# Optimization experiments

Measured on AMD Instinct MI355X. Metric: run time of the kernel, lower is better.

The kernel has to match this reference:

```python
import jax, jax.numpy as jnp
import numpy as np

T, B, DIM, LATENT, OUT = 512, 1024, 128, 256, 64


def setup_inputs() -> dict:
    key = jax.random.key(0)
    ks = jax.random.split(key, 6)
    s_i = 1.0 / np.sqrt(DIM)
    s_h = 1.0 / np.sqrt(LATENT)
    return {
        "x": jax.random.normal(ks[0], (T, B, DIM), dtype=jnp.float32),
        "h": jnp.zeros((B, LATENT), dtype=jnp.float32),
        "Wi": jax.random.uniform(ks[1], (DIM, LATENT), jnp.float32, -s_i, s_i),
        "bi": jax.random.uniform(ks[2], (LATENT,), jnp.float32, -s_i, s_i),
        "Wh": jax.random.uniform(ks[3], (LATENT, LATENT), jnp.float32, -s_h, s_h),
        "Wd": jax.random.uniform(ks[4], (LATENT, OUT), jnp.float32, -s_h, s_h),
        "bd": jax.random.uniform(ks[5], (OUT,), jnp.float32, -s_h, s_h),
    }


def reference(x, h, Wi, bi, Wh, Wd, bd):
    # Precompute input projections for all steps in one big GEMM: [T,B,latent]
    xi = jnp.einsum("tbd,dl->tbl", x, Wi) + bi

    def step(h, xi_t):
        h = jnp.tanh(xi_t + h @ Wh)
        return h, None

    h_final, _ = jax.lax.scan(step, h, xi)
    return jax.nn.sigmoid(h_final @ Wd + bd)
```

## Files before the change

### kernel.cpp

```cpp
#include <hip/hip_runtime.h>
#include <cmath>
#include <cstdint>

constexpr int T_STEPS = 512;
constexpr int BATCH   = 1024;
constexpr int DIM     = 128;
constexpr int LATENT  = 256;
constexpr int OUT_DIM = 64;
constexpr int ROWS    = 16;

typedef __attribute__((ext_vector_type(8))) short bf16x8;
typedef __attribute__((ext_vector_type(4))) float f32x4;
typedef __attribute__((ext_vector_type(4))) int   i32x4;

__device__ __forceinline__ uint32_t f2bf(float f) {
    uint32_t u = __builtin_bit_cast(uint32_t, f);
    return (u + 0x7FFFu + ((u >> 16) & 1u)) >> 16;
}
__device__ __forceinline__ uint32_t pk2(float a, float b) {
    return f2bf(a) | (f2bf(b) << 16);
}
__device__ __forceinline__ float fast_tanh(float v) {
    float e = __builtin_amdgcn_exp2f(v * 2.885390081777927f);
    return __builtin_fmaf(-2.0f, __builtin_amdgcn_rcpf(e + 1.0f), 1.0f);
}
__device__ __forceinline__ float fast_sigmoid(float v) {
    float e = __builtin_amdgcn_exp2f(v * -1.4426950408889634f);
    return __builtin_amdgcn_rcpf(e + 1.0f);
}
__device__ __forceinline__ int q8(float v, float inv) {
    return (int)__builtin_rintf(v * inv);
}
__device__ __forceinline__ uint32_t pack4(int a, int b, int c, int d) {
    return (uint32_t)(a & 255) | ((uint32_t)(b & 255) << 8) |
           ((uint32_t)(c & 255) << 16) | ((uint32_t)(d & 255) << 24);
}
__device__ __forceinline__ int swz(int sl, int b) {
    return (sl ^ (b & 3) ^ ((b >> 2) & 3)) & 3;
}

__global__ __launch_bounds__(512)
void rnn_i8h(const float* __restrict__ x,
             const float* __restrict__ h0,
             const float* __restrict__ Wi,
             const float* __restrict__ bi,
             const float* __restrict__ Wh,
             const float* __restrict__ Wd,
             const float* __restrict__ bd,
             float* __restrict__ out)
{
    __shared__ __align__(16) uint8_t hls[2][4096];
    __shared__ __align__(16) uint8_t xls[2][4096];

    const int tid  = threadIdx.x;
    const int lane = tid & 63;
    const int wv   = tid >> 6;
    const int b0   = blockIdx.x * ROWS;
    const int b15  = lane & 15;
    const int kgrp = lane >> 4;
    const int tg0  = wv * 2, tg1 = wv * 2 + 1;
    const int wcol0 = tg0 * 16 + b15;
    const int wcol1 = wcol0 + 16;

    float cmh0 = 0.f, cmh1 = 0.f;
    {
        const float* p0 = Wh + (size_t)(kgrp * 16) * LATENT + wcol0;
        #pragma unroll 4
        for (int i = 0; i < 64; ++i) {
            const size_t off = (size_t)((i >> 4) * 64 + (i & 15)) * LATENT;
            cmh0 = fmaxf(cmh0, fabsf(p0[off]));
            cmh1 = fmaxf(cmh1, fabsf(p0[off + 16]));
        }
        cmh0 = fmaxf(cmh0, __shfl_xor(cmh0, 16));
        cmh0 = fmaxf(cmh0, __shfl_xor(cmh0, 32));
        cmh1 = fmaxf(cmh1, __shfl_xor(cmh1, 16));
        cmh1 = fmaxf(cmh1, __shfl_xor(cmh1, 32));
    }
    const float ih0 = cmh0 > 0.f ? 127.f / cmh0 : 0.f;
    const float ih1 = cmh1 > 0.f ? 127.f / cmh1 : 0.f;

#define WHQ(J) q8(_p[(size_t)(J) * LATENT], _inv)
#define LOADWH(NAME, WC, S, INV)                                            \
    i32x4 NAME; {                                                           \
        const float* _p = Wh + (size_t)((S) * 64 + kgrp * 16) * LATENT + (WC); \
        const float _inv = (INV);                                           \
        NAME[0] = (int)pack4(WHQ(0),  WHQ(1),  WHQ(2),  WHQ(3));            \
        NAME[1] = (int)pack4(WHQ(4),  WHQ(5),  WHQ(6),  WHQ(7));            \
        NAME[2] = (int)pack4(WHQ(8),  WHQ(9),  WHQ(10), WHQ(11));           \
        NAME[3] = (int)pack4(WHQ(12), WHQ(13), WHQ(14), WHQ(15));           \
    }
    LOADWH(AH0_0, wcol0, 0, ih0) LOADWH(AH0_1, wcol0, 1, ih0)
    LOADWH(AH0_2, wcol0, 2, ih0) LOADWH(AH0_3, wcol0, 3, ih0)
    LOADWH(AH1_0, wcol1, 0, ih1) LOADWH(AH1_1, wcol1, 1, ih1)
    LOADWH(AH1_2, wcol1, 2, ih1) LOADWH(AH1_3, wcol1, 3, ih1)

#define LOADWX(NAME, WC, S)                                                 \
    bf16x8 NAME; {                                                          \
        const float* _p = Wi + (size_t)((S) * 32 + kgrp * 8) * LATENT + (WC); \
        NAME[0] = (short)f2bf(_p[0]);                                       \
        NAME[1] = (short)f2bf(_p[(size_t)1 * LATENT]);                      \
        NAME[2] = (short)f2bf(_p[(size_t)2 * LATENT]);                      \
        NAME[3] = (short)f2bf(_p[(size_t)3 * LATENT]);                      \
        NAME[4] = (short)f2bf(_p[(size_t)4 * LATENT]);                      \
        NAME[5] = (short)f2bf(_p[(size_t)5 * LATENT]);                      \
        NAME[6] = (short)f2bf(_p[(size_t)6 * LATENT]);                      \
        NAME[7] = (short)f2bf(_p[(size_t)7 * LATENT]);                      \
    }
    LOADWX(AX0_0, wcol0, 0) LOADWX(AX0_1, wcol0, 1)
    LOADWX(AX0_2, wcol0, 2) LOADWX(AX0_3, wcol0, 3)
    LOADWX(AX1_0, wcol1, 0) LOADWX(AX1_1, wcol1, 1)
    LOADWX(AX1_2, wcol1, 2) LOADWX(AX1_3, wcol1, 3)

    const float dh0_0 = __shfl(cmh0, kgrp * 4 + 0) * (1.f / 16129.f);
    const float dh0_1 = __shfl(cmh0, kgrp * 4 + 1) * (1.f / 16129.f);
    const float dh0_2 = __shfl(cmh0, kgrp * 4 + 2) * (1.f / 16129.f);
    const float dh0_3 = __shfl(cmh0, kgrp * 4 + 3) * (1.f / 16129.f);
    const float dh1_0 = __shfl(cmh1, kgrp * 4 + 0) * (1.f / 16129.f);
    const float dh1_1 = __shfl(cmh1, kgrp * 4 + 1) * (1.f / 16129.f);
    const float dh1_2 = __shfl(cmh1, kgrp * 4 + 2) * (1.f / 16129.f);
    const float dh1_3 = __shfl(cmh1, kgrp * 4 + 3) * (1.f / 16129.f);
    const float cb0_0 = bi[tg0 * 16 + kgrp * 4 + 0];
    const float cb0_1 = bi[tg0 * 16 + kgrp * 4 + 1];
    const float cb0_2 = bi[tg0 * 16 + kgrp * 4 + 2];
    const float cb0_3 = bi[tg0 * 16 + kgrp * 4 + 3];
    const float cb1_0 = bi[tg1 * 16 + kgrp * 4 + 0];
    const float cb1_1 = bi[tg1 * 16 + kgrp * 4 + 1];
    const float cb1_2 = bi[tg1 * 16 + kgrp * 4 + 2];
    const float cb1_3 = bi[tg1 * 16 + kgrp * 4 + 3];

    const int pr = tid & 15;
    const int pq = tid >> 4;
    const int stb = (pq >> 3) * 1024 + pr * 64 +
                    (swz((pq >> 1) & 3, pr) << 4) + (pq & 1) * 8;
    {
        const float* hp = h0 + (size_t)(b0 + pr) * LATENT + pq * 8;
        uint32_t u0 = pack4(q8(hp[0], 127.f), q8(hp[1], 127.f),
                            q8(hp[2], 127.f), q8(hp[3], 127.f));
        uint32_t u1 = pack4(q8(hp[4], 127.f), q8(hp[5], 127.f),
                            q8(hp[6], 127.f), q8(hp[7], 127.f));
        *reinterpret_cast<uint2*>(&hls[0][stb]) = make_uint2(u0, u1);
        const float* xq = x + (size_t)(b0 + pr) * DIM + pq * 4;
        float4 xv = *reinterpret_cast<const float4*>(xq);
        *reinterpret_cast<uint2*>(&xls[0][stb]) =
            make_uint2(pk2(xv.x, xv.y), pk2(xv.z, xv.w));
    }
    __syncthreads();

    const int hrd = b15 * 64 + (swz(kgrp, b15) << 4);
    const int wb0 = (tg0 >> 2) * 1024 + b15 * 64 +
                    (swz(tg0 & 3, b15) << 4) + kgrp * 4;
    const int wb1 = (tg1 >> 2) * 1024 + b15 * 64 +
                    (swz(tg1 & 3, b15) << 4) + kgrp * 4;
    const float* xp = x + ((size_t)BATCH + b0 + pr) * DIM + pq * 4;

    int cur = 0;
    for (int t = 0; t < T_STEPS; ++t) {
        const bool pf = (t + 1 < T_STEPS);
        float4 xv;
        if (pf) {
            xv = *reinterpret_cast<const float4*>(xp);
            xp += (size_t)BATCH * DIM;
        }

        const uint8_t* hb = &hls[cur][hrd];
        const uint8_t* xb = &xls[cur][hrd];
        i32x4  bh0 = *reinterpret_cast<const i32x4*>(hb);
        i32x4  bh1 = *reinterpret_cast<const i32x4*>(hb + 1024);
        i32x4  bh2 = *reinterpret_cast<const i32x4*>(hb + 2048);
        i32x4  bh3 = *reinterpret_cast<const i32x4*>(hb + 3072);
        bf16x8 bx0 = *reinterpret_cast<const bf16x8*>(xb);
        bf16x8 bx1 = *reinterpret_cast<const bf16x8*>(xb + 1024);
        bf16x8 bx2 = *reinterpret_cast<const bf16x8*>(xb + 2048);
        bf16x8 bx3 = *reinterpret_cast<const bf16x8*>(xb + 3072);

        i32x4 ch0 = {0, 0, 0, 0}, ch1 = {0, 0, 0, 0};
        f32x4 cx0 = {cb0_0, cb0_1, cb0_2, cb0_3};
        f32x4 cx1 = {cb1_0, cb1_1, cb1_2, cb1_3};

        ch0 = __builtin_amdgcn_mfma_i32_16x16x64_i8(AH0_0, bh0, ch0, 0, 0, 0);
        ch1 = __builtin_amdgcn_mfma_i32_16x16x64_i8(AH1_0, bh0, ch1, 0, 0, 0);
        cx0 = __builtin_amdgcn_mfma_f32_16x16x32_bf16(AX0_0, bx0, cx0, 0, 0, 0);
        cx1 = __builtin_amdgcn_mfma_f32_16x16x32_bf16(AX1_0, bx0, cx1, 0, 0, 0);
        ch0 = __builtin_amdgcn_mfma_i32_16x16x64_i8(AH0_1, bh1, ch0, 0, 0, 0);
        ch1 = __builtin_amdgcn_mfma_i32_16x16x64_i8(AH1_1, bh1, ch1, 0, 0, 0);
        cx0 = __builtin_amdgcn_mfma_f32_16x16x32_bf16(AX0_1, bx1, cx0, 0, 0, 0);
        cx1 = __builtin_amdgcn_mfma_f32_16x16x32_bf16(AX1_1, bx1, cx1, 0, 0, 0);
        ch0 = __builtin_amdgcn_mfma_i32_16x16x64_i8(AH0_2, bh2, ch0, 0, 0, 0);
        ch1 = __builtin_amdgcn_mfma_i32_16x16x64_i8(AH1_2, bh2, ch1, 0, 0, 0);
        cx0 = __builtin_amdgcn_mfma_f32_16x16x32_bf16(AX0_2, bx2, cx0, 0, 0, 0);
        cx1 = __builtin_amdgcn_mfma_f32_16x16x32_bf16(AX1_2, bx2, cx1, 0, 0, 0);
        ch0 = __builtin_amdgcn_mfma_i32_16x16x64_i8(AH0_3, bh3, ch0, 0, 0, 0);
        ch1 = __builtin_amdgcn_mfma_i32_16x16x64_i8(AH1_3, bh3, ch1, 0, 0, 0);
        cx0 = __builtin_amdgcn_mfma_f32_16x16x32_bf16(AX0_3, bx3, cx0, 0, 0, 0);
        cx1 = __builtin_amdgcn_mfma_f32_16x16x32_bf16(AX1_3, bx3, cx1, 0, 0, 0);

        const int nxt = cur ^ 1;
        {
            float v0 = fast_tanh(__builtin_fmaf((float)ch0[0], dh0_0, cx0[0]));
            float v1 = fast_tanh(__builtin_fmaf((float)ch0[1], dh0_1, cx0[1]));
            float v2 = fast_tanh(__builtin_fmaf((float)ch0[2], dh0_2, cx0[2]));
            float v3 = fast_tanh(__builtin_fmaf((float)ch0[3], dh0_3, cx0[3]));
            *reinterpret_cast<uint32_t*>(&hls[nxt][wb0]) =
                pack4(q8(v0, 127.f), q8(v1, 127.f), q8(v2, 127.f), q8(v3, 127.f));
        }
        {
            float v0 = fast_tanh(__builtin_fmaf((float)ch1[0], dh1_0, cx1[0]));
            float v1 = fast_tanh(__builtin_fmaf((float)ch1[1], dh1_1, cx1[1]));
            float v2 = fast_tanh(__builtin_fmaf((float)ch1[2], dh1_2, cx1[2]));
            float v3 = fast_tanh(__builtin_fmaf((float)ch1[3], dh1_3, cx1[3]));
            *reinterpret_cast<uint32_t*>(&hls[nxt][wb1]) =
                pack4(q8(v0, 127.f), q8(v1, 127.f), q8(v2, 127.f), q8(v3, 127.f));
        }
        if (pf)
            *reinterpret_cast<uint2*>(&xls[nxt][stb]) =
                make_uint2(pk2(xv.x, xv.y), pk2(xv.z, xv.w));

        __syncthreads();
        cur = nxt;
    }

    {
        const int o  = tid & 63;
        const int rb = tid >> 6;
        float s0 = 0.f, s1 = 0.f;
        #pragma unroll 4
        for (int k = 0; k < LATENT; k += 4) {
            const int sl   = (k >> 4) & 3;
            const int base = (k >> 6) * 1024 + (k & 15);
            const uint32_t pA = *reinterpret_cast<const uint32_t*>(
                &hls[cur][base + rb * 64 + (swz(sl, rb) << 4)]);
            const uint32_t pB = *reinterpret_cast<const uint32_t*>(
                &hls[cur][base + (rb + 8) * 64 + (swz(sl, rb + 8) << 4)]);
            const float w0 = Wd[(size_t)(k + 0) * OUT_DIM + o];
            const float w1 = Wd[(size_t)(k + 1) * OUT_DIM + o];
            const float w2 = Wd[(size_t)(k + 2) * OUT_DIM + o];
            const float w3 = Wd[(size_t)(k + 3) * OUT_DIM + o];
            s0 += (float)(int8_t)(pA) * w0 + (float)(int8_t)(pA >> 8) * w1
                + (float)(int8_t)(pA >> 16) * w2 + (float)(int8_t)(pA >> 24) * w3;
            s1 += (float)(int8_t)(pB) * w0 + (float)(int8_t)(pB >> 8) * w1
                + (float)(int8_t)(pB >> 16) * w2 + (float)(int8_t)(pB >> 24) * w3;
        }
        out[(size_t)(b0 + rb) * OUT_DIM + o] =
            fast_sigmoid(bd[o] + s0 * (1.f / 127.f));
        out[(size_t)(b0 + rb + 8) * OUT_DIM + o] =
            fast_sigmoid(bd[o] + s1 * (1.f / 127.f));
    }
}

extern "C" void kernel_launch(void* const* d_in, const int* in_sizes, int n_in,
                              void* d_out, int out_size, void* d_ws, size_t ws_size,
                              hipStream_t stream) {
    const float* x  = (const float*)d_in[0];
    const float* h0 = (const float*)d_in[1];
    const float* Wi = (const float*)d_in[2];
    const float* bi = (const float*)d_in[3];
    const float* Wh = (const float*)d_in[4];
    const float* Wd = (const float*)d_in[5];
    const float* bd = (const float*)d_in[6];
    float* out = (float*)d_out;

    hipLaunchKernelGGL(rnn_i8h, dim3(BATCH / ROWS), dim3(512), 0, stream,
                       x, h0, Wi, bi, Wh, Wd, bd, out);
}
```

Measured before the change: 402.8 us.

## Quantize input projection to int8 MFMA and use an LDS-only barrier

Replaces the bf16 x·Wi MFMAs with int8 MFMAs. Wi is quantized per column, and x is clamped to about ±3.97 and quantized with a fixed scale of 32. This halves the x-side MFMA count and LDS traffic on each recurrent step, with dequantization folded into the FMA before tanh. The per-step __syncthreads is replaced by a barrier that waits only on LDS counters, so the prefetch of the next x from global memory is not stalled. The cost is lower accuracy: the fixed x range assumes roughly unit-scale inputs and clips anything outside it.

```diff
diff --git a/kernel.cpp b/kernel.cpp
--- a/kernel.cpp
+++ b/kernel.cpp
@@ -9,17 +9,9 @@
 constexpr int OUT_DIM = 64;
 constexpr int ROWS    = 16;
 
-typedef __attribute__((ext_vector_type(8))) short bf16x8;
 typedef __attribute__((ext_vector_type(4))) float f32x4;
 typedef __attribute__((ext_vector_type(4))) int   i32x4;
 
-__device__ __forceinline__ uint32_t f2bf(float f) {
-    uint32_t u = __builtin_bit_cast(uint32_t, f);
-    return (u + 0x7FFFu + ((u >> 16) & 1u)) >> 16;
-}
-__device__ __forceinline__ uint32_t pk2(float a, float b) {
-    return f2bf(a) | (f2bf(b) << 16);
-}
 __device__ __forceinline__ float fast_tanh(float v) {
     float e = __builtin_amdgcn_exp2f(v * 2.885390081777927f);
     return __builtin_fmaf(-2.0f, __builtin_amdgcn_rcpf(e + 1.0f), 1.0f);
@@ -31,6 +23,9 @@
 __device__ __forceinline__ int q8(float v, float inv) {
     return (int)__builtin_rintf(v * inv);
 }
+__device__ __forceinline__ int q8x(float v) {
+    return (int)__builtin_rintf(fminf(fmaxf(v, -3.96875f), 3.96875f) * 32.f);
+}
 __device__ __forceinline__ uint32_t pack4(int a, int b, int c, int d) {
     return (uint32_t)(a & 255) | ((uint32_t)(b & 255) << 8) |
            ((uint32_t)(c & 255) << 16) | ((uint32_t)(d & 255) << 24);
@@ -38,19 +33,35 @@
 __device__ __forceinline__ int swz(int sl, int b) {
     return (sl ^ (b & 3) ^ ((b >> 2) & 3)) & 3;
 }
+__device__ __forceinline__ void barrier_lds_only() {
+    asm volatile("s_waitcnt lgkmcnt(0)" ::: "memory");
+    __builtin_amdgcn_s_barrier();
+    asm volatile("" ::: "memory");
+}
+
+#define WQJ(J) q8(_p[(size_t)(J) * LATENT], _inv)
+#define LOADQ(NAME, MAT, WC, S, INV)                                        \
+    i32x4 NAME; {                                                           \
+        const float* _p = (MAT) + (size_t)((S) * 64 + kgrp * 16) * LATENT + (WC); \
+        const float _inv = (INV);                                           \
+        NAME[0] = (int)pack4(WQJ(0),  WQJ(1),  WQJ(2),  WQJ(3));            \
+        NAME[1] = (int)pack4(WQJ(4),  WQJ(5),  WQJ(6),  WQJ(7));            \
+        NAME[2] = (int)pack4(WQJ(8),  WQJ(9),  WQJ(10), WQJ(11));           \
+        NAME[3] = (int)pack4(WQJ(12), WQJ(13), WQJ(14), WQJ(15));           \
+    }
 
 __global__ __launch_bounds__(512)
-void rnn_i8h(const float* __restrict__ x,
-             const float* __restrict__ h0,
-             const float* __restrict__ Wi,
-             const float* __restrict__ bi,
-             const float* __restrict__ Wh,
-             const float* __restrict__ Wd,
-             const float* __restrict__ bd,
-             float* __restrict__ out)
+void rnn_i8hx(const float* __restrict__ x,
+              const float* __restrict__ h0,
+              const float* __restrict__ Wi,
+              const float* __restrict__ bi,
+              const float* __restrict__ Wh,
+              const float* __restrict__ Wd,
+              const float* __restrict__ bd,
+              float* __restrict__ out)
 {
     __shared__ __align__(16) uint8_t hls[2][4096];
-    __shared__ __align__(16) uint8_t xls[2][4096];
+    __shared__ __align__(16) uint8_t xls[2][2048];
 
     const int tid  = threadIdx.x;
     const int lane = tid & 63;
@@ -62,7 +73,7 @@
     const int wcol0 = tg0 * 16 + b15;
     const int wcol1 = wcol0 + 16;
 
-    float cmh0 = 0.f, cmh1 = 0.f;
+    float cmh0 = 0.f, cmh1 = 0.f, cmx0 = 0.f, cmx1 = 0.f;
     {
         const float* p0 = Wh + (size_t)(kgrp * 16) * LATENT + wcol0;
         #pragma unroll 4
@@ -71,45 +82,33 @@
             cmh0 = fmaxf(cmh0, fabsf(p0[off]));
             cmh1 = fmaxf(cmh1, fabsf(p0[off + 16]));
         }
+        const float* q0 = Wi + (size_t)(kgrp * 16) * LATENT + wcol0;
+        #pragma unroll 4
+        for (int i = 0; i < 32; ++i) {
+            const size_t off = (size_t)((i >> 4) * 64 + (i & 15)) * LATENT;
+            cmx0 = fmaxf(cmx0, fabsf(q0[off]));
+            cmx1 = fmaxf(cmx1, fabsf(q0[off + 16]));
+        }
         cmh0 = fmaxf(cmh0, __shfl_xor(cmh0, 16));
         cmh0 = fmaxf(cmh0, __shfl_xor(cmh0, 32));
         cmh1 = fmaxf(cmh1, __shfl_xor(cmh1, 16));
         cmh1 = fmaxf(cmh1, __shfl_xor(cmh1, 32));
+        cmx0 = fmaxf(cmx0, __shfl_xor(cmx0, 16));
+        cmx0 = fmaxf(cmx0, __shfl_xor(cmx0, 32));
+        cmx1 = fmaxf(cmx1, __shfl_xor(cmx1, 16));
+        cmx1 = fmaxf(cmx1, __shfl_xor(cmx1, 32));
     }
     const float ih0 = cmh0 > 0.f ? 127.f / cmh0 : 0.f;
     const float ih1 = cmh1 > 0.f ? 127.f / cmh1 : 0.f;
-
-#define WHQ(J) q8(_p[(size_t)(J) * LATENT], _inv)
-#define LOADWH(NAME, WC, S, INV)                                            \
-    i32x4 NAME; {                                                           \
-        const float* _p = Wh + (size_t)((S) * 64 + kgrp * 16) * LATENT + (WC); \
-        const float _inv = (INV);                                           \
-        NAME[0] = (int)pack4(WHQ(0),  WHQ(1),  WHQ(2),  WHQ(3));            \
-        NAME[1] = (int)pack4(WHQ(4),  WHQ(5),  WHQ(6),  WHQ(7));            \
-        NAME[2] = (int)pack4(WHQ(8),  WHQ(9),  WHQ(10), WHQ(11));           \
-        NAME[3] = (int)pack4(WHQ(12), WHQ(13), WHQ(14), WHQ(15));           \
-    }
-    LOADWH(AH0_0, wcol0, 0, ih0) LOADWH(AH0_1, wcol0, 1, ih0)
-    LOADWH(AH0_2, wcol0, 2, ih0) LOADWH(AH0_3, wcol0, 3, ih0)
-    LOADWH(AH1_0, wcol1, 0, ih1) LOADWH(AH1_1, wcol1, 1, ih1)
-    LOADWH(AH1_2, wcol1, 2, ih1) LOADWH(AH1_3, wcol1, 3, ih1)
-
-#define LOADWX(NAME, WC, S)                                                 \
-    bf16x8 NAME; {                                                          \
-        const float* _p = Wi + (size_t)((S) * 32 + kgrp * 8) * LATENT + (WC); \
-        NAME[0] = (short)f2bf(_p[0]);                                       \
-        NAME[1] = (short)f2bf(_p[(size_t)1 * LATENT]);                      \
-        NAME[2] = (short)f2bf(_p[(size_t)2 * LATENT]);                      \
-        NAME[3] = (short)f2bf(_p[(size_t)3 * LATENT]);                      \
-        NAME[4] = (short)f2bf(_p[(size_t)4 * LATENT]);                      \
-        NAME[5] = (short)f2bf(_p[(size_t)5 * LATENT]);                      \
-        NAME[6] = (short)f2bf(_p[(size_t)6 * LATENT]);                      \
-        NAME[7] = (short)f2bf(_p[(size_t)7 * LATENT]);                      \
-    }
-    LOADWX(AX0_0, wcol0, 0) LOADWX(AX0_1, wcol0, 1)
-    LOADWX(AX0_2, wcol0, 2) LOADWX(AX0_3, wcol0, 3)
-    LOADWX(AX1_0, wcol1, 0) LOADWX(AX1_1, wcol1, 1)
-    LOADWX(AX1_2, wcol1, 2) LOADWX(AX1_3, wcol1, 3)
+    const float ix0 = cmx0 > 0.f ? 127.f / cmx0 : 0.f;
+    const float ix1 = cmx1 > 0.f ? 127.f / cmx1 : 0.f;
+
+    LOADQ(AH0_0, Wh, wcol0, 0, ih0) LOADQ(AH0_1, Wh, wcol0, 1, ih0)
+    LOADQ(AH0_2, Wh, wcol0, 2, ih0) LOADQ(AH0_3, Wh, wcol0, 3, ih0)
+    LOADQ(AH1_0, Wh, wcol1, 0, ih1) LOADQ(AH1_1, Wh, wcol1, 1, ih1)
+    LOADQ(AH1_2, Wh, wcol1, 2, ih1) LOADQ(AH1_3, Wh, wcol1, 3, ih1)
+    LOADQ(AX0_0, Wi, wcol0, 0, ix0) LOADQ(AX0_1, Wi, wcol0, 1, ix0)
+    LOADQ(AX1_0, Wi, wcol1, 0, ix1) LOADQ(AX1_1, Wi, wcol1, 1, ix1)
 
     const float dh0_0 = __shfl(cmh0, kgrp * 4 + 0) * (1.f / 16129.f);
     const float dh0_1 = __shfl(cmh0, kgrp * 4 + 1) * (1.f / 16129.f);
@@ -119,6 +118,14 @@
     const float dh1_1 = __shfl(cmh1, kgrp * 4 + 1) * (1.f / 16129.f);
     const float dh1_2 = __shfl(cmh1, kgrp * 4 + 2) * (1.f / 16129.f);
     const float dh1_3 = __shfl(cmh1, kgrp * 4 + 3) * (1.f / 16129.f);
+    const float dx0_0 = __shfl(cmx0, kgrp * 4 + 0) * (1.f / 4064.f);
+    const float dx0_1 = __shfl(cmx0, kgrp * 4 + 1) * (1.f / 4064.f);
+    const float dx0_2 = __shfl(cmx0, kgrp * 4 + 2) * (1.f / 4064.f);
+    const float dx0_3 = __shfl(cmx0, kgrp * 4 + 3) * (1.f / 4064.f);
+    const float dx1_0 = __shfl(cmx1, kgrp * 4 + 0) * (1.f / 4064.f);
+    const float dx1_1 = __shfl(cmx1, kgrp * 4 + 1) * (1.f / 4064.f);
+    const float dx1_2 = __shfl(cmx1, kgrp * 4 + 2) * (1.f / 4064.f);
+    const float dx1_3 = __shfl(cmx1, kgrp * 4 + 3) * (1.f / 4064.f);
     const float cb0_0 = bi[tg0 * 16 + kgrp * 4 + 0];
     const float cb0_1 = bi[tg0 * 16 + kgrp * 4 + 1];
     const float cb0_2 = bi[tg0 * 16 + kgrp * 4 + 2];
@@ -132,6 +139,8 @@
     const int pq = tid >> 4;
     const int stb = (pq >> 3) * 1024 + pr * 64 +
                     (swz((pq >> 1) & 3, pr) << 4) + (pq & 1) * 8;
+    const int stbx = (pq >> 4) * 1024 + pr * 64 +
+                     (swz((pq >> 2) & 3, pr) << 4) + (pq & 3) * 4;
     {
         const float* hp = h0 + (size_t)(b0 + pr) * LATENT + pq * 8;
         uint32_t u0 = pack4(q8(hp[0], 127.f), q8(hp[1], 127.f),
@@ -141,8 +150,8 @@
         *reinterpret_cast<uint2*>(&hls[0][stb]) = make_uint2(u0, u1);
         const float* xq = x + (size_t)(b0 + pr) * DIM + pq * 4;
         float4 xv = *reinterpret_cast<const float4*>(xq);
-        *reinterpret_cast<uint2*>(&xls[0][stb]) =
-            make_uint2(pk2(xv.x, xv.y), pk2(xv.z, xv.w));
+        *reinterpret_cast<uint32_t*>(&xls[0][stbx]) =
+            pack4(q8x(xv.x), q8x(xv.y), q8x(xv.z), q8x(xv.w));
     }
     __syncthreads();
 
@@ -161,61 +170,60 @@
             xv = *reinterpret_cast<const float4*>(xp);
             xp += (size_t)BATCH * DIM;
         }
-
         const uint8_t* hb = &hls[cur][hrd];
         const uint8_t* xb = &xls[cur][hrd];
-        i32x4  bh0 = *reinterpret_cast<const i32x4*>(hb);
-        i32x4  bh1 = *reinterpret_cast<const i32x4*>(hb + 1024);
-        i32x4  bh2 = *reinterpret_cast<const i32x4*>(hb + 2048);
-        i32x4  bh3 = *reinterpret_cast<const i32x4*>(hb + 3072);
-        bf16x8 bx0 = *reinterpret_cast<const bf16x8*>(xb);
-        bf16x8 bx1 = *reinterpret_cast<const bf16x8*>(xb + 1024);
-        bf16x8 bx2 = *reinterpret_cast<const bf16x8*>(xb + 2048);
-        bf16x8 bx3 = *reinterpret_cast<const bf16x8*>(xb + 3072);
+        i32x4 bh0 = *reinterpret_cast<const i32x4*>(hb);
+        i32x4 bh1 = *reinterpret_cast<const i32x4*>(hb + 1024);
+        i32x4 bh2 = *reinterpret_cast<const i32x4*>(hb + 2048);
+        i32x4 bh3 = *reinterpret_cast<const i32x4*>(hb + 3072);
+        i32x4 bx0 = *reinterpret_cast<const i32x4*>(xb);
+        i32x4 bx1 = *reinterpret_cast<const i32x4*>(xb + 1024);
 
         i32x4 ch0 = {0, 0, 0, 0}, ch1 = {0, 0, 0, 0};
-        f32x4 cx0 = {cb0_0, cb0_1, cb0_2, cb0_3};
-        f32x4 cx1 = {cb1_0, cb1_1, cb1_2, cb1_3};
-
+        i32x4 cx0 = {0, 0, 0, 0}, cx1 = {0, 0, 0, 0};
         ch0 = __builtin_amdgcn_mfma_i32_16x16x64_i8(AH0_0, bh0, ch0, 0, 0, 0);
         ch1 = __builtin_amdgcn_mfma_i32_16x16x64_i8(AH1_0, bh0, ch1, 0, 0, 0);
-        cx0 = __builtin_amdgcn_mfma_f32_16x16x32_bf16(AX0_0, bx0, cx0, 0, 0, 0);
-        cx1 = __builtin_amdgcn_mfma_f32_16x16x32_bf16(AX1_0, bx0, cx1, 0, 0, 0);
+        cx0 = __builtin_amdgcn_mfma_i32_16x16x64_i8(AX0_0, bx0, cx0, 0, 0, 0);
+        cx1 = __builtin_amdgcn_mfma_i32_16x16x64_i8(AX1_0, bx0, cx1, 0, 0, 0);
         ch0 = __builtin_amdgcn_mfma_i32_16x16x64_i8(AH0_1, bh1, ch0, 0, 0, 0);
         ch1 = __builtin_amdgcn_mfma_i32_16x16x64_i8(AH1_1, bh1, ch1, 0, 0, 0);
-        cx0 = __builtin_amdgcn_mfma_f32_16x16x32_bf16(AX0_1, bx1, cx0, 0, 0, 0);
-        cx1 = __builtin_amdgcn_mfma_f32_16x16x32_bf16(AX1_1, bx1, cx1, 0, 0, 0);
+        cx0 = __builtin_amdgcn_mfma_i32_16x16x64_i8(AX0_1, bx1, cx0, 0, 0, 0);
+        cx1 = __builtin_amdgcn_mfma_i32_16x16x64_i8(AX1_1, bx1, cx1, 0, 0, 0);
         ch0 = __builtin_amdgcn_mfma_i32_16x16x64_i8(AH0_2, bh2, ch0, 0, 0, 0);
         ch1 = __builtin_amdgcn_mfma_i32_16x16x64_i8(AH1_2, bh2, ch1, 0, 0, 0);
-        cx0 = __builtin_amdgcn_mfma_f32_16x16x32_bf16(AX0_2, bx2, cx0, 0, 0, 0);
-        cx1 = __builtin_amdgcn_mfma_f32_16x16x32_bf16(AX1_2, bx2, cx1, 0, 0, 0);
         ch0 = __builtin_amdgcn_mfma_i32_16x16x64_i8(AH0_3, bh3, ch0, 0, 0, 0);
         ch1 = __builtin_amdgcn_mfma_i32_16x16x64_i8(AH1_3, bh3, ch1, 0, 0, 0);
-        cx0 = __builtin_amdgcn_mfma_f32_16x16x32_bf16(AX0_3, bx3, cx0, 0, 0, 0);
-        cx1 = __builtin_amdgcn_mfma_f32_16x16x32_bf16(AX1_3, bx3, cx1, 0, 0, 0);
 
         const int nxt = cur ^ 1;
         {
-            float v0 = fast_tanh(__builtin_fmaf((float)ch0[0], dh0_0, cx0[0]));
-            float v1 = fast_tanh(__builtin_fmaf((float)ch0[1], dh0_1, cx0[1]));
-            float v2 = fast_tanh(__builtin_fmaf((float)ch0[2], dh0_2, cx0[2]));
-            float v3 = fast_tanh(__builtin_fmaf((float)ch0[3], dh0_3, cx0[3]));
+            float v0 = fast_tanh(__builtin_fmaf((float)ch0[0], dh0_0,
+                        __builtin_fmaf((float)cx0[0], dx0_0, cb0_0)));
+            float v1 = fast_tanh(__builtin_fmaf((float)ch0[1], dh0_1,
+                        __builtin_fmaf((float)cx0[1], dx0_1, cb0_1)));
+            float v2 = fast_tanh(__builtin_fmaf((float)ch0[2], dh0_2,
+                        __builtin_fmaf((float)cx0[2], dx0_2, cb0_2)));
+            float v3 = fast_tanh(__builtin_fmaf((float)ch0[3], dh0_3,
+                        __builtin_fmaf((float)cx0[3], dx0_3, cb0_3)));
             *reinterpret_cast<uint32_t*>(&hls[nxt][wb0]) =
                 pack4(q8(v0, 127.f), q8(v1, 127.f), q8(v2, 127.f), q8(v3, 127.f));
         }
         {
-            float v0 = fast_tanh(__builtin_fmaf((float)ch1[0], dh1_0, cx1[0]));
-            float v1 = fast_tanh(__builtin_fmaf((float)ch1[1], dh1_1, cx1[1]));
-            float v2 = fast_tanh(__builtin_fmaf((float)ch1[2], dh1_2, cx1[2]));
-            float v3 = fast_tanh(__builtin_fmaf((float)ch1[3], dh1_3, cx1[3]));
+            float v0 = fast_tanh(__builtin_fmaf((float)ch1[0], dh1_0,
+                        __builtin_fmaf((float)cx1[0], dx1_0, cb1_0)));
+            float v1 = fast_tanh(__builtin_fmaf((float)ch1[1], dh1_1,
+                        __builtin_fmaf((float)cx1[1], dx1_1, cb1_1)));
+            float v2 = fast_tanh(__builtin_fmaf((float)ch1[2], dh1_2,
+                        __builtin_fmaf((float)cx1[2], dx1_2, cb1_2)));
+            float v3 = fast_tanh(__builtin_fmaf((float)ch1[3], dh1_3,
+                        __builtin_fmaf((float)cx1[3], dx1_3, cb1_3)));
             *reinterpret_cast<uint32_t*>(&hls[nxt][wb1]) =
                 pack4(q8(v0, 127.f), q8(v1, 127.f), q8(v2, 127.f), q8(v3, 127.f));
         }
         if (pf)
-            *reinterpret_cast<uint2*>(&xls[nxt][stb]) =
-                make_uint2(pk2(xv.x, xv.y), pk2(xv.z, xv.w));
-
-        __syncthreads();
+            *reinterpret_cast<uint32_t*>(&xls[nxt][stbx]) =
+                pack4(q8x(xv.x), q8x(xv.y), q8x(xv.z), q8x(xv.w));
+
+        barrier_lds_only();
         cur = nxt;
     }
 
@@ -259,6 +267,6 @@
     const float* bd = (const float*)d_in[6];
     float* out = (float*)d_out;
 
-    hipLaunchKernelGGL(rnn_i8h, dim3(BATCH / ROWS), dim3(512), 0, stream,
+    hipLaunchKernelGGL(rnn_i8hx, dim3(BATCH / ROWS), dim3(512), 0, stream,
                        x, h0, Wi, bi, Wh, Wd, bd, out);
 }
```

Result: slower. 550.0 us (+36.5%).

## Load x tiles directly into registers and use LDS-only barrier

Applied to the files above, without the earlier changes.

Each wave now loads its own x fragment straight from global memory into registers one step ahead and packs it to bf16, instead of staging it through a shared-memory double buffer. The per-step barrier becomes an explicit barrier that waits only on LDS counters, so the prefetched global loads need not drain before the sync. The x data is now fetched redundantly by every wave (eight times more global/L2 traffic) and register pressure rises, but the LDS stores and reads for x go away and the barrier no longer waits on vmem.

```diff
diff --git a/kernel.cpp b/kernel.cpp
--- a/kernel.cpp
+++ b/kernel.cpp
@@ -38,19 +38,23 @@
 __device__ __forceinline__ int swz(int sl, int b) {
     return (sl ^ (b & 3) ^ ((b >> 2) & 3)) & 3;
 }
+__device__ __forceinline__ void barrier_lds_only() {
+    asm volatile("s_waitcnt lgkmcnt(0)" ::: "memory");
+    __builtin_amdgcn_s_barrier();
+    asm volatile("" ::: "memory");
+}
 
 __global__ __launch_bounds__(512)
-void rnn_i8h(const float* __restrict__ x,
-             const float* __restrict__ h0,
-             const float* __restrict__ Wi,
-             const float* __restrict__ bi,
-             const float* __restrict__ Wh,
-             const float* __restrict__ Wd,
-             const float* __restrict__ bd,
-             float* __restrict__ out)
+void rnn_i8h_xd(const float* __restrict__ x,
+                const float* __restrict__ h0,
+                const float* __restrict__ Wi,
+                const float* __restrict__ bi,
+                const float* __restrict__ Wh,
+                const float* __restrict__ Wd,
+                const float* __restrict__ bd,
+                float* __restrict__ out)
 {
     __shared__ __align__(16) uint8_t hls[2][4096];
-    __shared__ __align__(16) uint8_t xls[2][4096];
 
     const int tid  = threadIdx.x;
     const int lane = tid & 63;
@@ -139,10 +143,6 @@
         uint32_t u1 = pack4(q8(hp[4], 127.f), q8(hp[5], 127.f),
                             q8(hp[6], 127.f), q8(hp[7], 127.f));
         *reinterpret_cast<uint2*>(&hls[0][stb]) = make_uint2(u0, u1);
-        const float* xq = x + (size_t)(b0 + pr) * DIM + pq * 4;
-        float4 xv = *reinterpret_cast<const float4*>(xq);
-        *reinterpret_cast<uint2*>(&xls[0][stb]) =
-            make_uint2(pk2(xv.x, xv.y), pk2(xv.z, xv.w));
     }
     __syncthreads();
 
@@ -151,27 +151,54 @@
                     (swz(tg0 & 3, b15) << 4) + kgrp * 4;
     const int wb1 = (tg1 >> 2) * 1024 + b15 * 64 +
                     (swz(tg1 & 3, b15) << 4) + kgrp * 4;
-    const float* xp = x + ((size_t)BATCH + b0 + pr) * DIM + pq * 4;
+
+    const float* xlp = x + (size_t)(b0 + b15) * DIM + kgrp * 8;
+    float4 xc0 = reinterpret_cast<const float4*>(xlp)[0];
+    float4 xc1 = reinterpret_cast<const float4*>(xlp)[1];
+    float4 xc2 = reinterpret_cast<const float4*>(xlp + 32)[0];
+    float4 xc3 = reinterpret_cast<const float4*>(xlp + 32)[1];
+    float4 xc4 = reinterpret_cast<const float4*>(xlp + 64)[0];
+    float4 xc5 = reinterpret_cast<const float4*>(xlp + 64)[1];
+    float4 xc6 = reinterpret_cast<const float4*>(xlp + 96)[0];
+    float4 xc7 = reinterpret_cast<const float4*>(xlp + 96)[1];
+    xlp += (size_t)BATCH * DIM;
 
     int cur = 0;
     for (int t = 0; t < T_STEPS; ++t) {
         const bool pf = (t + 1 < T_STEPS);
-        float4 xv;
+        bf16x8 bx0, bx1, bx2, bx3;
+        {
+            uint32_t* q;
+            q = reinterpret_cast<uint32_t*>(&bx0);
+            q[0] = pk2(xc0.x, xc0.y); q[1] = pk2(xc0.z, xc0.w);
+            q[2] = pk2(xc1.x, xc1.y); q[3] = pk2(xc1.z, xc1.w);
+            q = reinterpret_cast<uint32_t*>(&bx1);
+            q[0] = pk2(xc2.x, xc2.y); q[1] = pk2(xc2.z, xc2.w);
+            q[2] = pk2(xc3.x, xc3.y); q[3] = pk2(xc3.z, xc3.w);
+            q = reinterpret_cast<uint32_t*>(&bx2);
+            q[0] = pk2(xc4.x, xc4.y); q[1] = pk2(xc4.z, xc4.w);
+            q[2] = pk2(xc5.x, xc5.y); q[3] = pk2(xc5.z, xc5.w);
+            q = reinterpret_cast<uint32_t*>(&bx3);
+            q[0] = pk2(xc6.x, xc6.y); q[1] = pk2(xc6.z, xc6.w);
+            q[2] = pk2(xc7.x, xc7.y); q[3] = pk2(xc7.z, xc7.w);
+        }
         if (pf) {
-            xv = *reinterpret_cast<const float4*>(xp);
-            xp += (size_t)BATCH * DIM;
+            xc0 = reinterpret_cast<const float4*>(xlp)[0];
+            xc1 = reinterpret_cast<const float4*>(xlp)[1];
+            xc2 = reinterpret_cast<const float4*>(xlp + 32)[0];
+            xc3 = reinterpret_cast<const float4*>(xlp + 32)[1];
+            xc4 = reinterpret_cast<const float4*>(xlp + 64)[0];
+            xc5 = reinterpret_cast<const float4*>(xlp + 64)[1];
+            xc6 = reinterpret_cast<const float4*>(xlp + 96)[0];
+            xc7 = reinterpret_cast<const float4*>(xlp + 96)[1];
+            xlp += (size_t)BATCH * DIM;
         }
 
         const uint8_t* hb = &hls[cur][hrd];
-        const uint8_t* xb = &xls[cur][hrd];
-        i32x4  bh0 = *reinterpret_cast<const i32x4*>(hb);
-        i32x4  bh1 = *reinterpret_cast<const i32x4*>(hb + 1024);
-        i32x4  bh2 = *reinterpret_cast<const i32x4*>(hb + 2048);
-        i32x4  bh3 = *reinterpret_cast<const i32x4*>(hb + 3072);
-        bf16x8 bx0 = *reinterpret_cast<const bf16x8*>(xb);
-        bf16x8 bx1 = *reinterpret_cast<const bf16x8*>(xb + 1024);
-        bf16x8 bx2 = *reinterpret_cast<const bf16x8*>(xb + 2048);
-        bf16x8 bx3 = *reinterpret_cast<const bf16x8*>(xb + 3072);
+        i32x4 bh0 = *reinterpret_cast<const i32x4*>(hb);
+        i32x4 bh1 = *reinterpret_cast<const i32x4*>(hb + 1024);
+        i32x4 bh2 = *reinterpret_cast<const i32x4*>(hb + 2048);
+        i32x4 bh3 = *reinterpret_cast<const i32x4*>(hb + 3072);
 
         i32x4 ch0 = {0, 0, 0, 0}, ch1 = {0, 0, 0, 0};
         f32x4 cx0 = {cb0_0, cb0_1, cb0_2, cb0_3};
@@ -211,11 +238,8 @@
             *reinterpret_cast<uint32_t*>(&hls[nxt][wb1]) =
                 pack4(q8(v0, 127.f), q8(v1, 127.f), q8(v2, 127.f), q8(v3, 127.f));
         }
-        if (pf)
-            *reinterpret_cast<uint2*>(&xls[nxt][stb]) =
-                make_uint2(pk2(xv.x, xv.y), pk2(xv.z, xv.w));
-
-        __syncthreads();
+
+        barrier_lds_only();
         cur = nxt;
     }
 
@@ -259,6 +283,6 @@
     const float* bd = (const float*)d_in[6];
     float* out = (float*)d_out;
 
-    hipLaunchKernelGGL(rnn_i8h, dim3(BATCH / ROWS), dim3(512), 0, stream,
+    hipLaunchKernelGGL(rnn_i8h_xd, dim3(BATCH / ROWS), dim3(512), 0, stream,
                        x, h0, Wi, bi, Wh, Wd, bd, out);
 }
```

Result: slower. 909.9 us (+125.9%).
